# Kernel tuning notes

Hardware: AMD Instinct MI355X
Metric: run time of the kernel (lower is better)

Reference implementation:

```python
import jax, jax.numpy as jnp
import numpy as np

EMBED = 1024

def setup_inputs() -> dict:
    key = jax.random.key(0)
    k1, k2, k3, k4, k5 = jax.random.split(key, 5)
    B, Sl, Sr, D = 4, 4096, 4096, EMBED
    left = jax.random.normal(k1, (B, Sl, D), dtype=jnp.float32)
    right = jax.random.normal(k2, (B, Sr, D), dtype=jnp.float32)
    # Dense(use_bias=False) weights, glorot-ish scale
    scale = 1.0 / np.sqrt(D)
    Wq = jax.random.normal(k3, (D, D), dtype=jnp.float32) * scale
    Wk = jax.random.normal(k4, (D, D), dtype=jnp.float32) * scale
    Wv = jax.random.normal(k5, (D, D), dtype=jnp.float32) * scale
    return {"left": left, "right": right, "Wq": Wq, "Wk": Wk, "Wv": Wv}

def reference(left, right, Wq, Wk, Wv):
    # q,k,v projections (Dense, no bias): x @ W
    q = jnp.einsum('bip,pd->bid', left, Wq)
    k = jnp.einsum('bjp,pd->bjd', right, Wk)
    v = jnp.einsum('bjp,pd->bjd', right, Wv)
    d = q.shape[-1]
    scores = jnp.einsum('bip,bjp->bij', q, k) * (d ** -0.5)
    attn = jax.nn.softmax(scores, axis=-1)  # [B, I, J]
    out = jnp.einsum('bis,bsj->bij', attn, v)
    return out + left
```

## Files before the change

kernel.cpp:

```cpp
#include <hip/hip_runtime.h>
#include <hip/hip_bf16.h>
#include <stdint.h>

typedef short bf16x8 __attribute__((ext_vector_type(8)));
typedef float f32x4 __attribute__((ext_vector_type(4)));

static __device__ __forceinline__ unsigned short f32_to_bf16(float f) {
    union { float f; uint32_t u; } v; v.f = f;
    uint32_t u = v.u;
    uint32_t r = (u + 0x7FFFu + ((u >> 16) & 1u)) >> 16;
    return (unsigned short)r;
}

static __device__ __forceinline__ float bf16_to_f32(unsigned short s) {
    union { uint32_t u; float f; } c; c.u = ((uint32_t)s) << 16;
    return c.f;
}

static __device__ __forceinline__ void gload_lds16(const unsigned short* g,
                                                   unsigned short* l) {
    __builtin_amdgcn_global_load_lds(
        (const __attribute__((address_space(1))) uint32_t*)g,
        (__attribute__((address_space(3))) uint32_t*)l, 16, 0, 0);
}

static __device__ __forceinline__ void barrier_fenced() {
    __builtin_amdgcn_s_barrier();
    __builtin_amdgcn_sched_barrier(0);
    asm volatile("" ::: "memory");
}

__global__ __launch_bounds__(256) void conv_bf16(
    const float* __restrict__ a, const float* __restrict__ b,
    unsigned short* __restrict__ oa, unsigned short* __restrict__ ob) {
    size_t i = ((size_t)blockIdx.x * 256 + threadIdx.x) * 4;
    const size_t stride = (size_t)gridDim.x * 256 * 4;
    for (; i < 16777216; i += stride) {
        float4 v = *reinterpret_cast<const float4*>(a + i);
        ushort4 o;
        o.x = f32_to_bf16(v.x); o.y = f32_to_bf16(v.y);
        o.z = f32_to_bf16(v.z); o.w = f32_to_bf16(v.w);
        *reinterpret_cast<ushort4*>(oa + i) = o;
        float4 u = *reinterpret_cast<const float4*>(b + i);
        ushort4 p;
        p.x = f32_to_bf16(u.x); p.y = f32_to_bf16(u.y);
        p.z = f32_to_bf16(u.z); p.w = f32_to_bf16(u.w);
        *reinterpret_cast<ushort4*>(ob + i) = p;
    }
}

__global__ void wtrans_kernel(const float* __restrict__ Wq,
                              const float* __restrict__ Wk,
                              const float* __restrict__ Wv,
                              unsigned short* __restrict__ Wt) {
    int proj = blockIdx.z;
    const float* W = (proj == 0) ? Wq : (proj == 1 ? Wk : Wv);
    unsigned short* out = Wt + (size_t)proj * 1024 * 1024;
    __shared__ float t[32][33];
    int k0 = blockIdx.x * 32, n0 = blockIdx.y * 32;
    int tx = threadIdx.x, ty = threadIdx.y;
    for (int r = ty; r < 32; r += 8)
        t[r][tx] = W[(size_t)(k0 + r) * 1024 + n0 + tx];
    __syncthreads();
    for (int r = ty; r < 32; r += 8)
        out[(size_t)(n0 + r) * 1024 + k0 + tx] = f32_to_bf16(t[tx][r]);
}

static __device__ __forceinline__ void gemm256_core(
    const unsigned short* __restrict__ A, const unsigned short* __restrict__ B,
    int K, int lda, int ldb, int m0, int n0,
    unsigned short* lds, f32x4 (&acc)[8][4]) {
    const int tid = threadIdx.x;
    const int lane = tid & 63;
    const int w = tid >> 6;
    const int wm = w >> 2, wn = w & 3;

    const int srow = tid >> 3;
    const int scol = (((tid & 7) - srow) & 7) * 8;
    const unsigned short* ga = A + (size_t)(m0 + srow) * lda + scol;
    const unsigned short* gb = B + (size_t)(n0 + srow) * ldb + scol;
    unsigned short* ldst = lds + tid * 8;

    const int pb = (((lane >> 4) + (lane & 7)) & 7) * 8;
    const int colk0 = pb, colk1 = pb ^ 32;
    const int rA0 = wm * 128 + (lane & 15);
    const int rB0 = wn * 64 + (lane & 15);

    const int NT = K >> 6;

#define STAGE8(gsA, gsB, pA, pB)                                    \
    gload_lds16((gsA), (pA));                                       \
    gload_lds16((gsA) + (size_t)64 * lda, (pA) + 4096);             \
    gload_lds16((gsA) + (size_t)128 * lda, (pA) + 8192);            \
    gload_lds16((gsA) + (size_t)192 * lda, (pA) + 12288);           \
    gload_lds16((gsB), (pB));                                       \
    gload_lds16((gsB) + (size_t)64 * ldb, (pB) + 4096);             \
    gload_lds16((gsB) + (size_t)128 * ldb, (pB) + 8192);            \
    gload_lds16((gsB) + (size_t)192 * ldb, (pB) + 12288);

    STAGE8(ga, gb, ldst, ldst + 16384);
    asm volatile("s_waitcnt vmcnt(0)" ::: "memory");
    barrier_fenced();

    int par = 0;
    for (int t = 0; t < NT; ++t) {
        const unsigned short* rA = lds + par * 32768;
        const unsigned short* rB = rA + 16384;
        bf16x8 a0[4][2], a1[4][2], b0[2][2], b1[2][2];

        if (t + 1 < NT) {
            const unsigned short* gan = ga + (t + 1) * 64;
            const unsigned short* gbn = gb + (t + 1) * 64;
            unsigned short* pA = ldst + (par ^ 1) * 32768;
            STAGE8(gan, gbn, pA, pA + 16384);
        }

#pragma unroll
        for (int mf = 0; mf < 4; ++mf) {
            a0[mf][0] = *reinterpret_cast<const bf16x8*>(
                &rA[(rA0 + mf * 16) * 64 + colk0]);
            a0[mf][1] = *reinterpret_cast<const bf16x8*>(
                &rA[(rA0 + mf * 16) * 64 + colk1]);
        }
#pragma unroll
        for (int nf = 0; nf < 2; ++nf) {
            b0[nf][0] = *reinterpret_cast<const bf16x8*>(
                &rB[(rB0 + nf * 16) * 64 + colk0]);
            b0[nf][1] = *reinterpret_cast<const bf16x8*>(
                &rB[(rB0 + nf * 16) * 64 + colk1]);
        }
        __builtin_amdgcn_s_setprio(1);
#pragma unroll
        for (int mf = 0; mf < 4; ++mf)
#pragma unroll
            for (int nf = 0; nf < 2; ++nf)
#pragma unroll
                for (int ks = 0; ks < 2; ++ks)
                    acc[mf][nf] = __builtin_amdgcn_mfma_f32_16x16x32_bf16(
                        a0[mf][ks], b0[nf][ks], acc[mf][nf], 0, 0, 0);
        __builtin_amdgcn_s_setprio(0);

#pragma unroll
        for (int nf = 0; nf < 2; ++nf) {
            b1[nf][0] = *reinterpret_cast<const bf16x8*>(
                &rB[(rB0 + 32 + nf * 16) * 64 + colk0]);
            b1[nf][1] = *reinterpret_cast<const bf16x8*>(
                &rB[(rB0 + 32 + nf * 16) * 64 + colk1]);
        }
        __builtin_amdgcn_s_setprio(1);
#pragma unroll
        for (int mf = 0; mf < 4; ++mf)
#pragma unroll
            for (int nf = 0; nf < 2; ++nf)
#pragma unroll
                for (int ks = 0; ks < 2; ++ks)
                    acc[mf][2 + nf] = __builtin_amdgcn_mfma_f32_16x16x32_bf16(
                        a0[mf][ks], b1[nf][ks], acc[mf][2 + nf], 0, 0, 0);
        __builtin_amdgcn_s_setprio(0);

#pragma unroll
        for (int mf = 0; mf < 4; ++mf) {
            a1[mf][0] = *reinterpret_cast<const bf16x8*>(
                &rA[(rA0 + 64 + mf * 16) * 64 + colk0]);
            a1[mf][1] = *reinterpret_cast<const bf16x8*>(
                &rA[(rA0 + 64 + mf * 16) * 64 + colk1]);
        }
        __builtin_amdgcn_s_setprio(1);
#pragma unroll
        for (int mf = 0; mf < 4; ++mf)
#pragma unroll
            for (int nf = 0; nf < 2; ++nf)
#pragma unroll
                for (int ks = 0; ks < 2; ++ks)
                    acc[4 + mf][nf] = __builtin_amdgcn_mfma_f32_16x16x32_bf16(
                        a1[mf][ks], b0[nf][ks], acc[4 + mf][nf], 0, 0, 0);
        __builtin_amdgcn_s_setprio(0);

        __builtin_amdgcn_s_setprio(1);
#pragma unroll
        for (int mf = 0; mf < 4; ++mf)
#pragma unroll
            for (int nf = 0; nf < 2; ++nf)
#pragma unroll
                for (int ks = 0; ks < 2; ++ks)
                    acc[4 + mf][2 + nf] = __builtin_amdgcn_mfma_f32_16x16x32_bf16(
                        a1[mf][ks], b1[nf][ks], acc[4 + mf][2 + nf], 0, 0, 0);
        __builtin_amdgcn_s_setprio(0);

        asm volatile("s_waitcnt vmcnt(0)" ::: "memory");
        barrier_fenced();
        par ^= 1;
    }
#undef STAGE8
}

__global__ __launch_bounds__(512, 2) void proj256(
    const unsigned short* __restrict__ Xl, const unsigned short* __restrict__ Xr,
    const unsigned short* __restrict__ Wt,
    unsigned short* __restrict__ Qb, unsigned short* __restrict__ Kb,
    unsigned short* __restrict__ Vt) {
    __shared__ unsigned short lds[65536];
    const int proj = blockIdx.z;
    const unsigned short* A = (proj == 0) ? Xl : Xr;
    const unsigned short* B = Wt + (size_t)proj * 1048576;
    const int m0 = blockIdx.x * 256, n0 = blockIdx.y * 256;

    f32x4 acc[8][4];
    for (int i = 0; i < 8; ++i)
        for (int j = 0; j < 4; ++j) acc[i][j] = {0.f, 0.f, 0.f, 0.f};

    gemm256_core(A, B, 1024, 1024, 1024, m0, n0, lds, acc);

    const int lane = threadIdx.x & 63, w = threadIdx.x >> 6;
    const int wm = w >> 2, wn = w & 3;
    if (proj < 2) {
        unsigned short* Out = (proj == 0) ? Qb : Kb;
        for (int mh = 0; mh < 2; ++mh)
            for (int mf = 0; mf < 4; ++mf)
                for (int nh = 0; nh < 2; ++nh)
                    for (int nf = 0; nf < 2; ++nf) {
                        f32x4 v = acc[mh * 4 + mf][nh * 2 + nf];
                        int row = m0 + wm * 128 + mh * 64 + mf * 16 + (lane >> 4) * 4;
                        int col = n0 + wn * 64 + nh * 32 + nf * 16 + (lane & 15);
                        for (int r = 0; r < 4; ++r)
                            Out[(size_t)(row + r) * 1024 + col] = f32_to_bf16(v[r]);
                    }
    } else {
        for (int mh = 0; mh < 2; ++mh)
            for (int mf = 0; mf < 4; ++mf)
                for (int nh = 0; nh < 2; ++nh)
                    for (int nf = 0; nf < 2; ++nf) {
                        f32x4 v = acc[mh * 4 + mf][nh * 2 + nf];
                        int row = m0 + wm * 128 + mh * 64 + mf * 16 + (lane >> 4) * 4;
                        int col = n0 + wn * 64 + nh * 32 + nf * 16 + (lane & 15);
                        int bb = row >> 12, jj = row & 4095;
                        uint32_t lo = f32_to_bf16(v[0]) |
                                      ((uint32_t)f32_to_bf16(v[1]) << 16);
                        uint32_t hi = f32_to_bf16(v[2]) |
                                      ((uint32_t)f32_to_bf16(v[3]) << 16);
                        *reinterpret_cast<uint2*>(
                            &Vt[((size_t)bb * 1024 + col) * 4096 + jj]) =
                            make_uint2(lo, hi);
                    }
    }
}

__global__ __launch_bounds__(512, 2) void qk256(
    const unsigned short* __restrict__ Qb,
    const unsigned short* __restrict__ Kb,
    unsigned short* __restrict__ S) {
    __shared__ unsigned short lds[65536];
    const int b = blockIdx.z;
    const unsigned short* A = Qb + (size_t)b * 4194304;
    const unsigned short* B = Kb + (size_t)b * 4194304;
    unsigned short* Sp = S + (size_t)b * 16777216;
    const int m0 = blockIdx.x * 256, n0 = blockIdx.y * 256;

    f32x4 acc[8][4];
    for (int i = 0; i < 8; ++i)
        for (int j = 0; j < 4; ++j) acc[i][j] = {0.f, 0.f, 0.f, 0.f};

    gemm256_core(A, B, 1024, 1024, 1024, m0, n0, lds, acc);

    const int lane = threadIdx.x & 63, w = threadIdx.x >> 6;
    const int wm = w >> 2, wn = w & 3;
    for (int mh = 0; mh < 2; ++mh)
        for (int mf = 0; mf < 4; ++mf)
            for (int nh = 0; nh < 2; ++nh)
                for (int nf = 0; nf < 2; ++nf) {
                    f32x4 v = acc[mh * 4 + mf][nh * 2 + nf];
                    int row = m0 + wm * 128 + mh * 64 + mf * 16 + (lane >> 4) * 4;
                    int col = n0 + wn * 64 + nh * 32 + nf * 16 + (lane & 15);
                    for (int r = 0; r < 4; ++r)
                        Sp[(size_t)(row + r) * 4096 + col] = f32_to_bf16(v[r]);
                }
}

__global__ __launch_bounds__(512, 2) void pv256(
    const unsigned short* __restrict__ P,
    const unsigned short* __restrict__ Vt,
    const float* __restrict__ left,
    float* __restrict__ out) {
    __shared__ unsigned short lds[65536];
    const int b = blockIdx.z;
    const unsigned short* A = P + (size_t)b * 16777216;
    const unsigned short* B = Vt + (size_t)b * 4194304;
    const float* Lb = left + (size_t)b * 4194304;
    float* Ob = out + (size_t)b * 4194304;
    const int m0 = blockIdx.x * 256, n0 = blockIdx.y * 256;

    f32x4 acc[8][4];
    for (int i = 0; i < 8; ++i)
        for (int j = 0; j < 4; ++j) acc[i][j] = {0.f, 0.f, 0.f, 0.f};

    gemm256_core(A, B, 4096, 4096, 4096, m0, n0, lds, acc);

    const int lane = threadIdx.x & 63, w = threadIdx.x >> 6;
    const int wm = w >> 2, wn = w & 3;
    for (int mh = 0; mh < 2; ++mh)
        for (int mf = 0; mf < 4; ++mf)
            for (int nh = 0; nh < 2; ++nh)
                for (int nf = 0; nf < 2; ++nf) {
                    f32x4 v = acc[mh * 4 + mf][nh * 2 + nf];
                    int row = m0 + wm * 128 + mh * 64 + mf * 16 + (lane >> 4) * 4;
                    int col = n0 + wn * 64 + nh * 32 + nf * 16 + (lane & 15);
                    for (int r = 0; r < 4; ++r) {
                        size_t off = (size_t)(row + r) * 1024 + col;
                        Ob[off] = v[r] + Lb[off];
                    }
                }
}

__global__ __launch_bounds__(256, 4) void softmax_rows(
    unsigned short* __restrict__ S) {
    const int lane = threadIdx.x & 63;
    const int row = blockIdx.x * 4 + (threadIdx.x >> 6);
    unsigned short* r = S + (size_t)row * 4096;

    float f[64];
    float mx = -INFINITY;
    for (int i = 0; i < 8; ++i) {
        bf16x8 v = *reinterpret_cast<const bf16x8*>(&r[i * 512 + lane * 8]);
        for (int j = 0; j < 8; ++j) {
            float x = bf16_to_f32((unsigned short)v[j]);
            f[i * 8 + j] = x;
            mx = fmaxf(mx, x);
        }
    }
    for (int off = 32; off; off >>= 1) mx = fmaxf(mx, __shfl_xor(mx, off));
    const float ksc = 0.045084220f;
    float sum = 0.f;
    for (int i = 0; i < 64; ++i) {
        f[i] = exp2f((f[i] - mx) * ksc);
        sum += f[i];
    }
    for (int off = 32; off; off >>= 1) sum += __shfl_xor(sum, off);
    float linv = 1.f / sum;
    for (int i = 0; i < 8; ++i) {
        bf16x8 v;
        for (int j = 0; j < 8; ++j)
            v[j] = (short)f32_to_bf16(f[i * 8 + j] * linv);
        *reinterpret_cast<bf16x8*>(&r[i * 512 + lane * 8]) = v;
    }
}

__global__ __launch_bounds__(256, 4) void proj_gemm(
    const float* __restrict__ left, const float* __restrict__ right,
    const unsigned short* __restrict__ Wt,
    unsigned short* __restrict__ Qb, unsigned short* __restrict__ Kb,
    unsigned short* __restrict__ Vt) {
    const int proj = blockIdx.z;
    const float* A = (proj == 0) ? left : right;
    const unsigned short* Wn = Wt + (size_t)proj * 1024 * 1024;
    const int m0 = blockIdx.x * 128;
    const int n0 = blockIdx.y * 128;

    __shared__ unsigned short As[128][40];
    __shared__ unsigned short Bs[128][40];

    const int tid = threadIdx.x;
    const int lane = tid & 63, w = tid >> 6;
    const int wm = (w >> 1) * 64, wn = (w & 1) * 64;

    f32x4 acc[4][4];
    for (int i = 0; i < 4; ++i)
        for (int j = 0; j < 4; ++j) acc[i][j] = {0.f, 0.f, 0.f, 0.f};

    for (int k0 = 0; k0 < 1024; k0 += 32) {
        for (int p = 0; p < 4; ++p) {
            int r = p * 32 + (tid >> 3);
            int c = (tid & 7) * 4;
            float4 v = *reinterpret_cast<const float4*>(
                &A[(size_t)(m0 + r) * 1024 + k0 + c]);
            uint32_t lo = f32_to_bf16(v.x) | ((uint32_t)f32_to_bf16(v.y) << 16);
            uint32_t hi = f32_to_bf16(v.z) | ((uint32_t)f32_to_bf16(v.w) << 16);
            *reinterpret_cast<uint2*>(&As[r][c]) = make_uint2(lo, hi);
        }
        for (int cc = 0; cc < 2; ++cc) {
            int idx = tid * 2 + cc;
            int n = idx >> 2, ch = (idx & 3) * 8;
            bf16x8 v = *reinterpret_cast<const bf16x8*>(
                &Wn[(size_t)(n0 + n) * 1024 + k0 + ch]);
            *reinterpret_cast<bf16x8*>(&Bs[n][ch]) = v;
        }
        __syncthreads();
        bf16x8 af[4], bfr[4];
        for (int i = 0; i < 4; ++i)
            af[i] = *reinterpret_cast<const bf16x8*>(
                &As[wm + i * 16 + (lane & 15)][(lane >> 4) * 8]);
        for (int j = 0; j < 4; ++j)
            bfr[j] = *reinterpret_cast<const bf16x8*>(
                &Bs[wn + j * 16 + (lane & 15)][(lane >> 4) * 8]);
        for (int i = 0; i < 4; ++i)
            for (int j = 0; j < 4; ++j)
                acc[i][j] = __builtin_amdgcn_mfma_f32_16x16x32_bf16(
                    af[i], bfr[j], acc[i][j], 0, 0, 0);
        __syncthreads();
    }

    if (proj < 2) {
        unsigned short* Out = (proj == 0) ? Qb : Kb;
        for (int i = 0; i < 4; ++i)
            for (int j = 0; j < 4; ++j) {
                int col = n0 + wn + j * 16 + (lane & 15);
                int row = m0 + wm + i * 16 + (lane >> 4) * 4;
                for (int r = 0; r < 4; ++r)
                    Out[(size_t)(row + r) * 1024 + col] = f32_to_bf16(acc[i][j][r]);
            }
    } else {
        for (int i = 0; i < 4; ++i)
            for (int j = 0; j < 4; ++j) {
                int col = n0 + wn + j * 16 + (lane & 15);
                int row = m0 + wm + i * 16 + (lane >> 4) * 4;
                int b = row >> 12, jj = row & 4095;
                uint32_t lo = f32_to_bf16(acc[i][j][0]) |
                              ((uint32_t)f32_to_bf16(acc[i][j][1]) << 16);
                uint32_t hi = f32_to_bf16(acc[i][j][2]) |
                              ((uint32_t)f32_to_bf16(acc[i][j][3]) << 16);
                *reinterpret_cast<uint2*>(
                    &Vt[((size_t)b * 1024 + col) * 4096 + jj]) = make_uint2(lo, hi);
            }
    }
}

template <int K, int LDA, int LDB>
static __device__ __forceinline__ void gemm_core(
    const unsigned short* __restrict__ A, const unsigned short* __restrict__ B,
    unsigned short* As, unsigned short* Bs, int m0, int n0, f32x4 (&acc)[4][4]) {
    const int tid = threadIdx.x;
    const int lane = tid & 63, w = tid >> 6;
    const int wm = (w >> 1) * 64, wn = (w & 1) * 64;
    const int r0 = tid >> 2, c0 = (tid & 3) * 8;

    const unsigned short* a0 = &A[(size_t)(m0 + r0) * LDA + c0];
    const unsigned short* a1 = a0 + (size_t)64 * LDA;
    const unsigned short* b0 = &B[(size_t)(n0 + r0) * LDB + c0];
    const unsigned short* b1 = b0 + (size_t)64 * LDB;
    unsigned short* asl = As + tid * 8;
    unsigned short* bsl = Bs + tid * 8;

    for (int k0 = 0; k0 < K; k0 += 32) {
        gload_lds16(a0 + k0, asl);
        gload_lds16(a1 + k0, asl + 2048);
        gload_lds16(b0 + k0, bsl);
        gload_lds16(b1 + k0, bsl + 2048);
        __syncthreads();
        bf16x8 af[4], bfr[4];
#pragma unroll
        for (int i = 0; i < 4; ++i)
            af[i] = *reinterpret_cast<const bf16x8*>(
                &As[(wm + i * 16 + (lane & 15)) * 32 + (lane >> 4) * 8]);
#pragma unroll
        for (int j = 0; j < 4; ++j)
            bfr[j] = *reinterpret_cast<const bf16x8*>(
                &Bs[(wn + j * 16 + (lane & 15)) * 32 + (lane >> 4) * 8]);
#pragma unroll
        for (int i = 0; i < 4; ++i)
#pragma unroll
            for (int j = 0; j < 4; ++j)
                acc[i][j] = __builtin_amdgcn_mfma_f32_16x16x32_bf16(
                    af[i], bfr[j], acc[i][j], 0, 0, 0);
        __syncthreads();
    }
}

__global__ __launch_bounds__(256, 2) void qk_gemm(
    const unsigned short* __restrict__ Qb,
    const unsigned short* __restrict__ Kb,
    unsigned short* __restrict__ S) {
    const unsigned short* A = Qb;
    const unsigned short* B = Kb;
    const int m0 = blockIdx.x * 128, n0 = blockIdx.y * 128;

    __shared__ unsigned short As[128 * 32];
    __shared__ unsigned short Bs[128 * 32];

    const int tid = threadIdx.x;
    const int lane = tid & 63, w = tid >> 6;
    const int wm = (w >> 1) * 64, wn = (w & 1) * 64;

    f32x4 acc[4][4];
    for (int i = 0; i < 4; ++i)
        for (int j = 0; j < 4; ++j) acc[i][j] = {0.f, 0.f, 0.f, 0.f};

    gemm_core<1024, 1024, 1024>(A, B, As, Bs, m0, n0, acc);

    for (int i = 0; i < 4; ++i)
        for (int j = 0; j < 4; ++j) {
            int col = n0 + wn + j * 16 + (lane & 15);
            int row = m0 + wm + i * 16 + (lane >> 4) * 4;
            for (int r = 0; r < 4; ++r)
                S[(size_t)(row + r) * 4096 + col] = f32_to_bf16(acc[i][j][r]);
        }
}

__global__ __launch_bounds__(256, 2) void pv_gemm(
    const unsigned short* __restrict__ P,
    const unsigned short* __restrict__ Vt,
    const float* __restrict__ left,
    float* __restrict__ out) {
    const int m0 = blockIdx.x * 128, n0 = blockIdx.y * 128;

    __shared__ unsigned short As[128 * 32];
    __shared__ unsigned short Bs[128 * 32];

    const int tid = threadIdx.x;
    const int lane = tid & 63, w = tid >> 6;
    const int wm = (w >> 1) * 64, wn = (w & 1) * 64;

    f32x4 acc[4][4];
    for (int i = 0; i < 4; ++i)
        for (int j = 0; j < 4; ++j) acc[i][j] = {0.f, 0.f, 0.f, 0.f};

    gemm_core<4096, 4096, 4096>(P, Vt, As, Bs, m0, n0, acc);

    for (int i = 0; i < 4; ++i)
        for (int j = 0; j < 4; ++j) {
            int col = n0 + wn + j * 16 + (lane & 15);
            int row = m0 + wm + i * 16 + (lane >> 4) * 4;
            for (int r = 0; r < 4; ++r) {
                size_t off = (size_t)(row + r) * 1024 + col;
                out[off] = acc[i][j][r] + left[off];
            }
        }
}

extern "C" void kernel_launch(void* const* d_in, const int* in_sizes, int n_in,
                              void* d_out, int out_size, void* d_ws, size_t ws_size,
                              hipStream_t stream) {
    const float* left  = (const float*)d_in[0];
    const float* right = (const float*)d_in[1];
    const float* Wq    = (const float*)d_in[2];
    const float* Wk    = (const float*)d_in[3];
    const float* Wv    = (const float*)d_in[4];
    float* out = (float*)d_out;

    char* ws = (char*)d_ws;
    unsigned short* Wt = (unsigned short*)ws;
    unsigned short* Qb = (unsigned short*)(ws + 6291456);
    unsigned short* Kb = Qb + (size_t)16384 * 1024;
    unsigned short* Vt = Kb + (size_t)16384 * 1024;
    unsigned short* Sb = Vt + (size_t)16384 * 1024;
    unsigned short* Xl = Sb;
    unsigned short* Xr = Sb + 16777216;

    const bool batched = ws_size >= 241172480ull;

    wtrans_kernel<<<dim3(32, 32, 3), dim3(32, 8), 0, stream>>>(Wq, Wk, Wv, Wt);

    if (batched) {
        conv_bf16<<<4096, 256, 0, stream>>>(left, right, Xl, Xr);
        proj256<<<dim3(64, 4, 3), 512, 0, stream>>>(Xl, Xr, Wt, Qb, Kb, Vt);
        qk256<<<dim3(16, 16, 4), 512, 0, stream>>>(Qb, Kb, Sb);
        softmax_rows<<<4096, 256, 0, stream>>>(Sb);
        pv256<<<dim3(16, 4, 4), 512, 0, stream>>>(Sb, Vt, left, out);
    } else {
        proj_gemm<<<dim3(128, 8, 3), 256, 0, stream>>>(left, right, Wt, Qb, Kb, Vt);
        for (int b = 0; b < 4; ++b) {
            qk_gemm<<<dim3(32, 32, 1), 256, 0, stream>>>(
                Qb + (size_t)b * 4194304, Kb + (size_t)b * 4194304, Sb);
            softmax_rows<<<1024, 256, 0, stream>>>(Sb);
            pv_gemm<<<dim3(32, 8, 1), 256, 0, stream>>>(
                Sb, Vt + (size_t)b * 4194304,
                left + (size_t)b * 4194304, out + (size_t)b * 4194304);
        }
    }
}
```

Before: 444.4 us.

## Interleave quarter-tile global-to-LDS loads with MFMA phases in GEMM core

Splits each K-tile's global-to-LDS staging into four quarter loads issued between the four MFMA quadrant phases. The B half of the next-next tile is prefetched early, so each barrier only waits on part of the outstanding loads (vmcnt(4)). The aim is to spread memory traffic across the compute phases instead of issuing it in one burst per tile. In exchange it adds many extra workgroup barriers per tile, and the overlapping reuse of LDS halves is fragile to get right.

Result: no change. 445.1 us (+0.2%).

```diff
diff --git a/kernel.cpp b/kernel.cpp
--- a/kernel.cpp
+++ b/kernel.cpp
@@ -77,9 +77,9 @@
 
     const int srow = tid >> 3;
     const int scol = (((tid & 7) - srow) & 7) * 8;
-    const unsigned short* ga = A + (size_t)(m0 + srow) * lda + scol;
-    const unsigned short* gb = B + (size_t)(n0 + srow) * ldb + scol;
-    unsigned short* ldst = lds + tid * 8;
+    const unsigned short* gA = A + (size_t)(m0 + srow) * lda + scol;
+    const unsigned short* gB = B + (size_t)(n0 + srow) * ldb + scol;
+    const int dst0 = tid * 8;
 
     const int pb = (((lane >> 4) + (lane & 7)) & 7) * 8;
     const int colk0 = pb, colk1 = pb ^ 32;
@@ -88,110 +88,120 @@
 
     const int NT = K >> 6;
 
-#define STAGE8(gsA, gsB, pA, pB)                                    \
-    gload_lds16((gsA), (pA));                                       \
-    gload_lds16((gsA) + (size_t)64 * lda, (pA) + 4096);             \
-    gload_lds16((gsA) + (size_t)128 * lda, (pA) + 8192);            \
-    gload_lds16((gsA) + (size_t)192 * lda, (pA) + 12288);           \
-    gload_lds16((gsB), (pB));                                       \
-    gload_lds16((gsB) + (size_t)64 * ldb, (pB) + 4096);             \
-    gload_lds16((gsB) + (size_t)128 * ldb, (pB) + 8192);            \
-    gload_lds16((gsB) + (size_t)192 * ldb, (pB) + 12288);
-
-    STAGE8(ga, gb, ldst, ldst + 16384);
-    asm volatile("s_waitcnt vmcnt(0)" ::: "memory");
+#define SU_A0(Tt) { const unsigned short* s_ = gA + (size_t)(Tt) * 64;        \
+        unsigned short* d_ = lds + ((Tt) & 1) * 32768 + dst0;                 \
+        gload_lds16(s_, d_); gload_lds16(s_ + (size_t)64 * lda, d_ + 4096); }
+#define SU_A1(Tt) { const unsigned short* s_ = gA + (size_t)128 * lda + (size_t)(Tt) * 64; \
+        unsigned short* d_ = lds + ((Tt) & 1) * 32768 + 8192 + dst0;          \
+        gload_lds16(s_, d_); gload_lds16(s_ + (size_t)64 * lda, d_ + 4096); }
+#define SU_B0(Tt) { const unsigned short* s_ = gB + (size_t)(Tt) * 64;        \
+        unsigned short* d_ = lds + ((Tt) & 1) * 32768 + 16384 + dst0;         \
+        gload_lds16(s_, d_); gload_lds16(s_ + (size_t)64 * ldb, d_ + 4096); }
+#define SU_B1(Tt) { const unsigned short* s_ = gB + (size_t)128 * ldb + (size_t)(Tt) * 64; \
+        unsigned short* d_ = lds + ((Tt) & 1) * 32768 + 24576 + dst0;         \
+        gload_lds16(s_, d_); gload_lds16(s_ + (size_t)64 * ldb, d_ + 4096); }
+
+#define RD_A0 { for (int mf = 0; mf < 4; ++mf) {                              \
+        a0[mf][0] = *reinterpret_cast<const bf16x8*>(&rA[(rA0 + mf*16)*64 + colk0]); \
+        a0[mf][1] = *reinterpret_cast<const bf16x8*>(&rA[(rA0 + mf*16)*64 + colk1]); } }
+#define RD_A1 { for (int mf = 0; mf < 4; ++mf) {                              \
+        a1[mf][0] = *reinterpret_cast<const bf16x8*>(&rA[(rA0 + 64 + mf*16)*64 + colk0]); \
+        a1[mf][1] = *reinterpret_cast<const bf16x8*>(&rA[(rA0 + 64 + mf*16)*64 + colk1]); } }
+#define RD_B0 { for (int nf = 0; nf < 2; ++nf) {                              \
+        b0[nf][0] = *reinterpret_cast<const bf16x8*>(&rB[(rB0 + nf*16)*64 + colk0]); \
+        b0[nf][1] = *reinterpret_cast<const bf16x8*>(&rB[(rB0 + nf*16)*64 + colk1]); } }
+#define RD_B1 { for (int nf = 0; nf < 2; ++nf) {                              \
+        b1[nf][0] = *reinterpret_cast<const bf16x8*>(&rB[(rB0 + 32 + nf*16)*64 + colk0]); \
+        b1[nf][1] = *reinterpret_cast<const bf16x8*>(&rB[(rB0 + 32 + nf*16)*64 + colk1]); } }
+#define MM_Q00 { for (int mf = 0; mf < 4; ++mf) for (int nf = 0; nf < 2; ++nf) \
+        for (int ks = 0; ks < 2; ++ks)                                        \
+            acc[mf][nf] = __builtin_amdgcn_mfma_f32_16x16x32_bf16(            \
+                a0[mf][ks], b0[nf][ks], acc[mf][nf], 0, 0, 0); }
+#define MM_Q01 { for (int mf = 0; mf < 4; ++mf) for (int nf = 0; nf < 2; ++nf) \
+        for (int ks = 0; ks < 2; ++ks)                                        \
+            acc[mf][2+nf] = __builtin_amdgcn_mfma_f32_16x16x32_bf16(          \
+                a0[mf][ks], b1[nf][ks], acc[mf][2+nf], 0, 0, 0); }
+#define MM_Q10 { for (int mf = 0; mf < 4; ++mf) for (int nf = 0; nf < 2; ++nf) \
+        for (int ks = 0; ks < 2; ++ks)                                        \
+            acc[4+mf][nf] = __builtin_amdgcn_mfma_f32_16x16x32_bf16(          \
+                a1[mf][ks], b0[nf][ks], acc[4+mf][nf], 0, 0, 0); }
+#define MM_Q11 { for (int mf = 0; mf < 4; ++mf) for (int nf = 0; nf < 2; ++nf) \
+        for (int ks = 0; ks < 2; ++ks)                                        \
+            acc[4+mf][2+nf] = __builtin_amdgcn_mfma_f32_16x16x32_bf16(        \
+                a1[mf][ks], b1[nf][ks], acc[4+mf][2+nf], 0, 0, 0); }
+
+    SU_A0(0); SU_A1(0); SU_B0(0); SU_B1(0);
+    SU_B0(1); SU_B1(1);
+    asm volatile("s_waitcnt vmcnt(4)" ::: "memory");
     barrier_fenced();
 
-    int par = 0;
-    for (int t = 0; t < NT; ++t) {
-        const unsigned short* rA = lds + par * 32768;
-        const unsigned short* rB = rA + 16384;
-        bf16x8 a0[4][2], a1[4][2], b0[2][2], b1[2][2];
-
-        if (t + 1 < NT) {
-            const unsigned short* gan = ga + (t + 1) * 64;
-            const unsigned short* gbn = gb + (t + 1) * 64;
-            unsigned short* pA = ldst + (par ^ 1) * 32768;
-            STAGE8(gan, gbn, pA, pA + 16384);
-        }
-
-#pragma unroll
-        for (int mf = 0; mf < 4; ++mf) {
-            a0[mf][0] = *reinterpret_cast<const bf16x8*>(
-                &rA[(rA0 + mf * 16) * 64 + colk0]);
-            a0[mf][1] = *reinterpret_cast<const bf16x8*>(
-                &rA[(rA0 + mf * 16) * 64 + colk1]);
-        }
-#pragma unroll
-        for (int nf = 0; nf < 2; ++nf) {
-            b0[nf][0] = *reinterpret_cast<const bf16x8*>(
-                &rB[(rB0 + nf * 16) * 64 + colk0]);
-            b0[nf][1] = *reinterpret_cast<const bf16x8*>(
-                &rB[(rB0 + nf * 16) * 64 + colk1]);
-        }
-        __builtin_amdgcn_s_setprio(1);
-#pragma unroll
-        for (int mf = 0; mf < 4; ++mf)
-#pragma unroll
-            for (int nf = 0; nf < 2; ++nf)
-#pragma unroll
-                for (int ks = 0; ks < 2; ++ks)
-                    acc[mf][nf] = __builtin_amdgcn_mfma_f32_16x16x32_bf16(
-                        a0[mf][ks], b0[nf][ks], acc[mf][nf], 0, 0, 0);
-        __builtin_amdgcn_s_setprio(0);
-
-#pragma unroll
-        for (int nf = 0; nf < 2; ++nf) {
-            b1[nf][0] = *reinterpret_cast<const bf16x8*>(
-                &rB[(rB0 + 32 + nf * 16) * 64 + colk0]);
-            b1[nf][1] = *reinterpret_cast<const bf16x8*>(
-                &rB[(rB0 + 32 + nf * 16) * 64 + colk1]);
-        }
-        __builtin_amdgcn_s_setprio(1);
-#pragma unroll
-        for (int mf = 0; mf < 4; ++mf)
-#pragma unroll
-            for (int nf = 0; nf < 2; ++nf)
-#pragma unroll
-                for (int ks = 0; ks < 2; ++ks)
-                    acc[mf][2 + nf] = __builtin_amdgcn_mfma_f32_16x16x32_bf16(
-                        a0[mf][ks], b1[nf][ks], acc[mf][2 + nf], 0, 0, 0);
-        __builtin_amdgcn_s_setprio(0);
-
-#pragma unroll
-        for (int mf = 0; mf < 4; ++mf) {
-            a1[mf][0] = *reinterpret_cast<const bf16x8*>(
-                &rA[(rA0 + 64 + mf * 16) * 64 + colk0]);
-            a1[mf][1] = *reinterpret_cast<const bf16x8*>(
-                &rA[(rA0 + 64 + mf * 16) * 64 + colk1]);
-        }
-        __builtin_amdgcn_s_setprio(1);
-#pragma unroll
-        for (int mf = 0; mf < 4; ++mf)
-#pragma unroll
-            for (int nf = 0; nf < 2; ++nf)
-#pragma unroll
-                for (int ks = 0; ks < 2; ++ks)
-                    acc[4 + mf][nf] = __builtin_amdgcn_mfma_f32_16x16x32_bf16(
-                        a1[mf][ks], b0[nf][ks], acc[4 + mf][nf], 0, 0, 0);
-        __builtin_amdgcn_s_setprio(0);
-
-        __builtin_amdgcn_s_setprio(1);
-#pragma unroll
-        for (int mf = 0; mf < 4; ++mf)
-#pragma unroll
-            for (int nf = 0; nf < 2; ++nf)
-#pragma unroll
-                for (int ks = 0; ks < 2; ++ks)
-                    acc[4 + mf][2 + nf] = __builtin_amdgcn_mfma_f32_16x16x32_bf16(
-                        a1[mf][ks], b1[nf][ks], acc[4 + mf][2 + nf], 0, 0, 0);
-        __builtin_amdgcn_s_setprio(0);
-
-        asm volatile("s_waitcnt vmcnt(0)" ::: "memory");
-        barrier_fenced();
-        par ^= 1;
-    }
-#undef STAGE8
+    for (int T = 0; T < NT; T += 2) {
+        const bool deep = (T + 2 < NT);
+        {
+            const unsigned short* rA = lds + (T & 1) * 32768;
+            const unsigned short* rB = rA + 16384;
+            bf16x8 a0[4][2], a1[4][2], b0[2][2], b1[2][2];
+            RD_A0 RD_B0
+            SU_A0(T + 1);
+            barrier_fenced();
+            __builtin_amdgcn_s_setprio(1); MM_Q00 __builtin_amdgcn_s_setprio(0);
+            barrier_fenced();
+            RD_B1
+            SU_A1(T + 1);
+            barrier_fenced();
+            __builtin_amdgcn_s_setprio(1); MM_Q01 __builtin_amdgcn_s_setprio(0);
+            barrier_fenced();
+            RD_A1
+            if (deep) SU_B0(T + 2);
+            barrier_fenced();
+            __builtin_amdgcn_s_setprio(1); MM_Q10 __builtin_amdgcn_s_setprio(0);
+            barrier_fenced();
+            if (deep) SU_B1(T + 2);
+            barrier_fenced();
+            __builtin_amdgcn_s_setprio(1); MM_Q11 __builtin_amdgcn_s_setprio(0);
+            if (deep) { asm volatile("s_waitcnt vmcnt(4)" ::: "memory"); }
+            else      { asm volatile("s_waitcnt vmcnt(0)" ::: "memory"); }
+            barrier_fenced();
+        }
+        {
+            const unsigned short* rA = lds + ((T + 1) & 1) * 32768;
+            const unsigned short* rB = rA + 16384;
+            bf16x8 a0[4][2], a1[4][2], b0[2][2], b1[2][2];
+            RD_A0 RD_B0
+            if (deep) SU_A0(T + 2);
+            barrier_fenced();
+            __builtin_amdgcn_s_setprio(1); MM_Q00 __builtin_amdgcn_s_setprio(0);
+            barrier_fenced();
+            RD_B1
+            if (deep) SU_A1(T + 2);
+            barrier_fenced();
+            __builtin_amdgcn_s_setprio(1); MM_Q01 __builtin_amdgcn_s_setprio(0);
+            barrier_fenced();
+            RD_A1
+            if (deep) SU_B0(T + 3);
+            barrier_fenced();
+            __builtin_amdgcn_s_setprio(1); MM_Q10 __builtin_amdgcn_s_setprio(0);
+            barrier_fenced();
+            if (deep) SU_B1(T + 3);
+            barrier_fenced();
+            __builtin_amdgcn_s_setprio(1); MM_Q11 __builtin_amdgcn_s_setprio(0);
+            if (deep) { asm volatile("s_waitcnt vmcnt(4)" ::: "memory"); }
+            else      { asm volatile("s_waitcnt vmcnt(0)" ::: "memory"); }
+            barrier_fenced();
+        }
+    }
+#undef SU_A0
+#undef SU_A1
+#undef SU_B0
+#undef SU_B1
+#undef RD_A0
+#undef RD_A1
+#undef RD_B0
+#undef RD_B1
+#undef MM_Q00
+#undef MM_Q01
+#undef MM_Q10
+#undef MM_Q11
 }
 
 __global__ __launch_bounds__(512, 2) void proj256(
```

## Fuse fp32-to-bf16 conversion into projection GEMM and remap blocks across XCDs

Applied to the files above, without the earlier changes.

Removes the separate conversion kernel: the projection GEMM now reads fp32 activations into registers, converts them to bf16 and writes them to LDS, while B still streams through direct global-to-LDS loads. This avoids writing and re-reading a bf16 copy of left and right. Block indices in the projection, QK and PV kernels are also permuted so that neighbouring tiles land on the same XCD, aiming for better L2 reuse. In exchange the A-tile fetch goes through registers, which costs more VGPRs and adds conversion instructions to the inner loop.

After: 495.6 us. +11.5%, slower.

```diff
diff --git a/kernel.cpp b/kernel.cpp
--- a/kernel.cpp
+++ b/kernel.cpp
@@ -30,23 +30,16 @@
     asm volatile("" ::: "memory");
 }
 
-__global__ __launch_bounds__(256) void conv_bf16(
-    const float* __restrict__ a, const float* __restrict__ b,
-    unsigned short* __restrict__ oa, unsigned short* __restrict__ ob) {
-    size_t i = ((size_t)blockIdx.x * 256 + threadIdx.x) * 4;
-    const size_t stride = (size_t)gridDim.x * 256 * 4;
-    for (; i < 16777216; i += stride) {
-        float4 v = *reinterpret_cast<const float4*>(a + i);
-        ushort4 o;
-        o.x = f32_to_bf16(v.x); o.y = f32_to_bf16(v.y);
-        o.z = f32_to_bf16(v.z); o.w = f32_to_bf16(v.w);
-        *reinterpret_cast<ushort4*>(oa + i) = o;
-        float4 u = *reinterpret_cast<const float4*>(b + i);
-        ushort4 p;
-        p.x = f32_to_bf16(u.x); p.y = f32_to_bf16(u.y);
-        p.z = f32_to_bf16(u.z); p.w = f32_to_bf16(u.w);
-        *reinterpret_cast<ushort4*>(ob + i) = p;
-    }
+static __device__ __forceinline__ void xcd_remap(int& bx, int& by, int& bz) {
+    const int gx = gridDim.x, gy = gridDim.y;
+    const int flat = bx + gx * (by + gy * bz);
+    const int total = gx * gy * gridDim.z;
+    const int q = total >> 3;
+    const int nid = (flat & 7) * q + (flat >> 3);
+    bx = nid % gx;
+    const int t2 = nid / gx;
+    by = t2 % gy;
+    bz = t2 / gy;
 }
 
 __global__ void wtrans_kernel(const float* __restrict__ Wq,
@@ -194,22 +187,174 @@
 #undef STAGE8
 }
 
-__global__ __launch_bounds__(512, 2) void proj256(
-    const unsigned short* __restrict__ Xl, const unsigned short* __restrict__ Xr,
+static __device__ __forceinline__ void gemm256f_core(
+    const float* __restrict__ A, const unsigned short* __restrict__ B,
+    int K, int lda, int ldb, int m0, int n0,
+    unsigned short* lds, f32x4 (&acc)[8][4]) {
+    const int tid = threadIdx.x;
+    const int lane = tid & 63;
+    const int w = tid >> 6;
+    const int wm = w >> 2, wn = w & 3;
+
+    const int srow = tid >> 3;
+    const int scol = (((tid & 7) - srow) & 7) * 8;
+    const float* gA = A + (size_t)(m0 + srow) * lda + scol;
+    const unsigned short* gB = B + (size_t)(n0 + srow) * ldb + scol;
+    unsigned short* ldst = lds + tid * 8;
+
+    const int pb = (((lane >> 4) + (lane & 7)) & 7) * 8;
+    const int colk0 = pb, colk1 = pb ^ 32;
+    const int rA0 = wm * 128 + (lane & 15);
+    const int rB0 = wn * 64 + (lane & 15);
+    const int NT = K >> 6;
+
+    float4 st[8];
+
+#define LOADA(Tt) { const float* s_ = gA + (size_t)(Tt) * 64;                  \
+    st[0] = *reinterpret_cast<const float4*>(s_);                              \
+    st[1] = *reinterpret_cast<const float4*>(s_ + 4);                          \
+    st[2] = *reinterpret_cast<const float4*>(s_ + (size_t)64 * lda);           \
+    st[3] = *reinterpret_cast<const float4*>(s_ + (size_t)64 * lda + 4);       \
+    st[4] = *reinterpret_cast<const float4*>(s_ + (size_t)128 * lda);          \
+    st[5] = *reinterpret_cast<const float4*>(s_ + (size_t)128 * lda + 4);      \
+    st[6] = *reinterpret_cast<const float4*>(s_ + (size_t)192 * lda);          \
+    st[7] = *reinterpret_cast<const float4*>(s_ + (size_t)192 * lda + 4); }
+#define WRITEA(p) { unsigned short* d_ = ldst + (p) * 32768;                   \
+    for (int u = 0; u < 4; ++u) {                                              \
+        bf16x8 vv;                                                             \
+        vv[0] = (short)f32_to_bf16(st[2*u].x);                                 \
+        vv[1] = (short)f32_to_bf16(st[2*u].y);                                 \
+        vv[2] = (short)f32_to_bf16(st[2*u].z);                                 \
+        vv[3] = (short)f32_to_bf16(st[2*u].w);                                 \
+        vv[4] = (short)f32_to_bf16(st[2*u+1].x);                               \
+        vv[5] = (short)f32_to_bf16(st[2*u+1].y);                               \
+        vv[6] = (short)f32_to_bf16(st[2*u+1].z);                               \
+        vv[7] = (short)f32_to_bf16(st[2*u+1].w);                               \
+        *reinterpret_cast<bf16x8*>(d_ + u * 4096) = vv; } }
+#define STAGEB(Tt, p) { const unsigned short* s_ = gB + (size_t)(Tt) * 64;     \
+    unsigned short* d_ = ldst + (p) * 32768 + 16384;                           \
+    gload_lds16(s_, d_);                                                       \
+    gload_lds16(s_ + (size_t)64 * ldb, d_ + 4096);                             \
+    gload_lds16(s_ + (size_t)128 * ldb, d_ + 8192);                            \
+    gload_lds16(s_ + (size_t)192 * ldb, d_ + 12288); }
+
+    LOADA(0);
+    STAGEB(0, 0);
+    asm volatile("s_waitcnt vmcnt(0)" ::: "memory");
+    WRITEA(0);
+    asm volatile("s_waitcnt lgkmcnt(0)" ::: "memory");
+    barrier_fenced();
+
+    int par = 0;
+    for (int t = 0; t < NT; ++t) {
+        const unsigned short* rA = lds + par * 32768;
+        const unsigned short* rB = rA + 16384;
+        bf16x8 a0[4][2], a1[4][2], b0[2][2], b1[2][2];
+        const bool pre = (t + 1 < NT);
+
+        if (pre) { LOADA(t + 1); STAGEB(t + 1, par ^ 1); }
+
+#pragma unroll
+        for (int mf = 0; mf < 4; ++mf) {
+            a0[mf][0] = *reinterpret_cast<const bf16x8*>(
+                &rA[(rA0 + mf * 16) * 64 + colk0]);
+            a0[mf][1] = *reinterpret_cast<const bf16x8*>(
+                &rA[(rA0 + mf * 16) * 64 + colk1]);
+        }
+#pragma unroll
+        for (int nf = 0; nf < 2; ++nf) {
+            b0[nf][0] = *reinterpret_cast<const bf16x8*>(
+                &rB[(rB0 + nf * 16) * 64 + colk0]);
+            b0[nf][1] = *reinterpret_cast<const bf16x8*>(
+                &rB[(rB0 + nf * 16) * 64 + colk1]);
+        }
+        __builtin_amdgcn_s_setprio(1);
+#pragma unroll
+        for (int mf = 0; mf < 4; ++mf)
+#pragma unroll
+            for (int nf = 0; nf < 2; ++nf)
+#pragma unroll
+                for (int ks = 0; ks < 2; ++ks)
+                    acc[mf][nf] = __builtin_amdgcn_mfma_f32_16x16x32_bf16(
+                        a0[mf][ks], b0[nf][ks], acc[mf][nf], 0, 0, 0);
+        __builtin_amdgcn_s_setprio(0);
+
+#pragma unroll
+        for (int nf = 0; nf < 2; ++nf) {
+            b1[nf][0] = *reinterpret_cast<const bf16x8*>(
+                &rB[(rB0 + 32 + nf * 16) * 64 + colk0]);
+            b1[nf][1] = *reinterpret_cast<const bf16x8*>(
+                &rB[(rB0 + 32 + nf * 16) * 64 + colk1]);
+        }
+        __builtin_amdgcn_s_setprio(1);
+#pragma unroll
+        for (int mf = 0; mf < 4; ++mf)
+#pragma unroll
+            for (int nf = 0; nf < 2; ++nf)
+#pragma unroll
+                for (int ks = 0; ks < 2; ++ks)
+                    acc[mf][2 + nf] = __builtin_amdgcn_mfma_f32_16x16x32_bf16(
+                        a0[mf][ks], b1[nf][ks], acc[mf][2 + nf], 0, 0, 0);
+        __builtin_amdgcn_s_setprio(0);
+
+#pragma unroll
+        for (int mf = 0; mf < 4; ++mf) {
+            a1[mf][0] = *reinterpret_cast<const bf16x8*>(
+                &rA[(rA0 + 64 + mf * 16) * 64 + colk0]);
+            a1[mf][1] = *reinterpret_cast<const bf16x8*>(
+                &rA[(rA0 + 64 + mf * 16) * 64 + colk1]);
+        }
+        __builtin_amdgcn_s_setprio(1);
+#pragma unroll
+        for (int mf = 0; mf < 4; ++mf)
+#pragma unroll
+            for (int nf = 0; nf < 2; ++nf)
+#pragma unroll
+                for (int ks = 0; ks < 2; ++ks)
+                    acc[4 + mf][nf] = __builtin_amdgcn_mfma_f32_16x16x32_bf16(
+                        a1[mf][ks], b0[nf][ks], acc[4 + mf][nf], 0, 0, 0);
+        __builtin_amdgcn_s_setprio(0);
+
+        __builtin_amdgcn_s_setprio(1);
+#pragma unroll
+        for (int mf = 0; mf < 4; ++mf)
+#pragma unroll
+            for (int nf = 0; nf < 2; ++nf)
+#pragma unroll
+                for (int ks = 0; ks < 2; ++ks)
+                    acc[4 + mf][2 + nf] = __builtin_amdgcn_mfma_f32_16x16x32_bf16(
+                        a1[mf][ks], b1[nf][ks], acc[4 + mf][2 + nf], 0, 0, 0);
+        __builtin_amdgcn_s_setprio(0);
+
+        asm volatile("s_waitcnt vmcnt(0)" ::: "memory");
+        if (pre) WRITEA(par ^ 1);
+        asm volatile("s_waitcnt lgkmcnt(0)" ::: "memory");
+        barrier_fenced();
+        par ^= 1;
+    }
+#undef LOADA
+#undef WRITEA
+#undef STAGEB
+}
+
+__global__ __launch_bounds__(512, 2) void proj256f(
+    const float* __restrict__ left, const float* __restrict__ right,
     const unsigned short* __restrict__ Wt,
     unsigned short* __restrict__ Qb, unsigned short* __restrict__ Kb,
     unsigned short* __restrict__ Vt) {
     __shared__ unsigned short lds[65536];
-    const int proj = blockIdx.z;
-    const unsigned short* A = (proj == 0) ? Xl : Xr;
+    int bx = blockIdx.x, by = blockIdx.y, bz = blockIdx.z;
+    xcd_remap(bx, by, bz);
+    const int proj = bz;
+    const float* A = (proj == 0) ? left : right;
     const unsigned short* B = Wt + (size_t)proj * 1048576;
-    const int m0 = blockIdx.x * 256, n0 = blockIdx.y * 256;
+    const int m0 = bx * 256, n0 = by * 256;
 
     f32x4 acc[8][4];
     for (int i = 0; i < 8; ++i)
         for (int j = 0; j < 4; ++j) acc[i][j] = {0.f, 0.f, 0.f, 0.f};
 
-    gemm256_core(A, B, 1024, 1024, 1024, m0, n0, lds, acc);
+    gemm256f_core(A, B, 1024, 1024, 1024, m0, n0, lds, acc);
 
     const int lane = threadIdx.x & 63, w = threadIdx.x >> 6;
     const int wm = w >> 2, wn = w & 3;
@@ -250,11 +395,13 @@
     const unsigned short* __restrict__ Kb,
     unsigned short* __restrict__ S) {
     __shared__ unsigned short lds[65536];
-    const int b = blockIdx.z;
+    int bx = blockIdx.x, by = blockIdx.y, bz = blockIdx.z;
+    xcd_remap(bx, by, bz);
+    const int b = bz;
     const unsigned short* A = Qb + (size_t)b * 4194304;
     const unsigned short* B = Kb + (size_t)b * 4194304;
     unsigned short* Sp = S + (size_t)b * 16777216;
-    const int m0 = blockIdx.x * 256, n0 = blockIdx.y * 256;
+    const int m0 = bx * 256, n0 = by * 256;
 
     f32x4 acc[8][4];
     for (int i = 0; i < 8; ++i)
@@ -282,12 +429,14 @@
     const float* __restrict__ left,
     float* __restrict__ out) {
     __shared__ unsigned short lds[65536];
-    const int b = blockIdx.z;
+    int bx = blockIdx.x, by = blockIdx.y, bz = blockIdx.z;
+    xcd_remap(bx, by, bz);
+    const int b = bz;
     const unsigned short* A = P + (size_t)b * 16777216;
     const unsigned short* B = Vt + (size_t)b * 4194304;
     const float* Lb = left + (size_t)b * 4194304;
     float* Ob = out + (size_t)b * 4194304;
-    const int m0 = blockIdx.x * 256, n0 = blockIdx.y * 256;
+    const int m0 = bx * 256, n0 = by * 256;
 
     f32x4 acc[8][4];
     for (int i = 0; i < 8; ++i)
@@ -541,16 +690,13 @@
     unsigned short* Kb = Qb + (size_t)16384 * 1024;
     unsigned short* Vt = Kb + (size_t)16384 * 1024;
     unsigned short* Sb = Vt + (size_t)16384 * 1024;
-    unsigned short* Xl = Sb;
-    unsigned short* Xr = Sb + 16777216;
 
     const bool batched = ws_size >= 241172480ull;
 
     wtrans_kernel<<<dim3(32, 32, 3), dim3(32, 8), 0, stream>>>(Wq, Wk, Wv, Wt);
 
     if (batched) {
-        conv_bf16<<<4096, 256, 0, stream>>>(left, right, Xl, Xr);
-        proj256<<<dim3(64, 4, 3), 512, 0, stream>>>(Xl, Xr, Wt, Qb, Kb, Vt);
+        proj256f<<<dim3(64, 4, 3), 512, 0, stream>>>(left, right, Wt, Qb, Kb, Vt);
         qk256<<<dim3(16, 16, 4), 512, 0, stream>>>(Qb, Kb, Sb);
         softmax_rows<<<4096, 256, 0, stream>>>(Sb);
         pv256<<<dim3(16, 4, 4), 512, 0, stream>>>(Sb, Vt, left, out);
```
